# Kernel tuning notes

Measured on AMD Instinct MI355X. Metric: run time of the kernel, lower is better.

Reference implementation:

```python
import jax, jax.numpy as jnp
import numpy as np

SEQ_LEN, INPUT_DIM, HIDDEN_DIM, OUTPUT_DIM = 1024, 128, 256, 128
BATCH = 256


def setup_inputs() -> dict:
    key = jax.random.key(0)
    ks = jax.random.split(key, 7)
    s_ih = 1.0 / np.sqrt(INPUT_DIM)
    s_hh = 1.0 / np.sqrt(HIDDEN_DIM)
    return {
        "x": jax.random.normal(ks[0], (BATCH, SEQ_LEN, INPUT_DIM), jnp.float32),
        "W_ih": jax.random.normal(ks[1], (INPUT_DIM, 4 * HIDDEN_DIM), jnp.float32) * s_ih,
        "W_hh": jax.random.normal(ks[2], (HIDDEN_DIM, 4 * HIDDEN_DIM), jnp.float32) * s_hh,
        "b_ih": jax.random.normal(ks[3], (4 * HIDDEN_DIM,), jnp.float32) * s_hh,
        "b_hh": jax.random.normal(ks[4], (4 * HIDDEN_DIM,), jnp.float32) * s_hh,
        "W_out": jax.random.normal(ks[5], (HIDDEN_DIM, OUTPUT_DIM), jnp.float32) * s_hh,
        "b_out": jax.random.normal(ks[6], (OUTPUT_DIM,), jnp.float32) * s_hh,
    }


def reference(x, W_ih, W_hh, b_ih, b_hh, W_out, b_out):
    B, T, _ = x.shape
    H = W_hh.shape[0]
    # Precompute input projections for all timesteps: [T, B, 4H]
    x_proj = jnp.einsum("bti,ig->tbg", x, W_ih) + (b_ih + b_hh)

    def step(carry, xp_t):
        h, c = carry
        gates = xp_t + h @ W_hh  # [B, 4H]
        i_t, f_t, g_t, o_t = jnp.split(gates, 4, axis=1)
        i_t = jax.nn.sigmoid(i_t)
        f_t = jax.nn.sigmoid(f_t)
        g_t = jnp.tanh(g_t)
        o_t = jax.nn.sigmoid(o_t)
        c = f_t * c + i_t * g_t
        h = o_t * jnp.tanh(c)
        return (h, c), None

    h0 = jnp.zeros((B, H), x.dtype)
    c0 = jnp.zeros((B, H), x.dtype)
    (h_T, _), _ = jax.lax.scan(step, (h0, c0), x_proj)
    return h_T @ W_out + b_out
```

## Files before the change

### kernel.cpp

```cpp
#include <hip/hip_runtime.h>
#include <cstdint>


#define T_    1024
#define I_    128
#define H_    256

typedef short s8v __attribute__((ext_vector_type(8)));
typedef float f4v __attribute__((ext_vector_type(4)));
typedef unsigned short u16;
typedef unsigned int   u32;
typedef unsigned long long u64;

__device__ __forceinline__ u16 f2bf(float f) {
  union { float f; u32 u; } v; v.f = f;
  u32 r = v.u + 0x7FFFu + ((v.u >> 16) & 1u);
  return (u16)(r >> 16);
}
__device__ __forceinline__ float bf2f(u16 h) {
  union { u32 u; float f; } v; v.u = ((u32)h) << 16;
  return v.f;
}
__device__ __forceinline__ float sig_(float x)  { return 1.0f / (1.0f + __expf(-x)); }
__device__ __forceinline__ float tanh_(float x) { return 2.0f / (1.0f + __expf(-2.0f * x)) - 1.0f; }

__device__ __forceinline__ void unpack8(const u64 w[4], s8v& hi, s8v& lo) {
  #pragma unroll
  for (int j = 0; j < 4; j++) {
    u32 a = (u32)w[j], b = (u32)(w[j] >> 32);
    hi[2*j]   = (short)(u16)a;        lo[2*j]   = (short)(u16)(a >> 16);
    hi[2*j+1] = (short)(u16)b;        lo[2*j+1] = (short)(u16)(b >> 16);
  }
}

__device__ __forceinline__ bool tagok(u64 w, u32 tag) {
  return ((((u32)(w >> 16)) & 3u) == tag) & ((((u32)(w >> 48)) & 3u) == tag);
}

__device__ __forceinline__ void lgkm_barrier() {
  asm volatile("s_waitcnt lgkmcnt(0)" ::: "memory");
  __builtin_amdgcn_sched_barrier(0);
  __builtin_amdgcn_s_barrier();
  __builtin_amdgcn_sched_barrier(0);
  asm volatile("" ::: "memory");
}

__global__ __launch_bounds__(256, 1) void lstm_persist(
    const float* __restrict__ x, const float* __restrict__ Wih,
    const float* __restrict__ Whh, const float* __restrict__ bih,
    const float* __restrict__ bhh, const float* __restrict__ Wout,
    const float* __restrict__ bout, float* __restrict__ out,
    u32* __restrict__ flags, u32* __restrict__ hbuf)
{
  (void)flags;
  const int bid  = blockIdx.x;
  const int xcd  = bid & 7;
  const int slot = bid >> 3;
  const int ct   = slot & 15;
  const int g    = ((slot >> 4) << 3) | xcd;
  const int tid  = threadIdx.x;
  const int wave = tid >> 6;
  const int lane = tid & 63;
  const int lm   = lane & 15;
  const int lq   = lane >> 4;

  __shared__ u16   Wlds[2][64][392];
  __shared__ u16   xlds[2][2][16][136];
  __shared__ float partial[4][4][16][20];

  const int cm  = tid >> 4;
  const int chc = tid & 15;

  const size_t hpar   = (size_t)16 * 16 * 256;
  const size_t hgbase = (size_t)g * 16 * 256;

  {
    u32* hz = hbuf + hgbase + (size_t)cm * 256 + ct * 16 + chc;
    __hip_atomic_store(hz,        0x00010000u, __ATOMIC_RELAXED, __HIP_MEMORY_SCOPE_AGENT);
    __hip_atomic_store(hz + hpar, 0u,          __ATOMIC_RELAXED, __HIP_MEMORY_SCOPE_AGENT);
  }

  for (int it = tid; it < 384 * 64; it += 256) {
    int k = it >> 6;
    int c = it & 63;
    int gcol = (c >> 4) * 256 + ct * 16 + (c & 15);
    float w = (k < 128) ? Wih[k * 1024 + gcol] : Whh[(k - 128) * 1024 + gcol];
    u16 hi = f2bf(w);
    Wlds[0][c][k] = hi;
    Wlds[1][c][k] = f2bf(w - bf2f(hi));
  }
  __syncthreads();

  s8v wfrag[3][4][2];
  #pragma unroll
  for (int ki = 0; ki < 3; ki++) {
    const int kt = wave + 4 * ki;
    #pragma unroll
    for (int gg = 0; gg < 4; gg++) {
      #pragma unroll
      for (int p = 0; p < 2; p++)
        wfrag[ki][gg][p] = *(const s8v*)&Wlds[p][gg * 16 + lm][kt * 32 + lq * 8];
    }
  }
  __syncthreads();

  float biasv[4];
  #pragma unroll
  for (int gg = 0; gg < 4; gg++) {
    int col = gg * 256 + ct * 16 + chc;
    biasv[gg] = bih[col] + bhh[col];
  }
  float cstate = 0.0f;

  const int xr  = tid >> 4;
  const int xc0 = (tid & 15) * 8;
  const float* xbase = x + (size_t)(g * 16 + xr) * (T_ * I_) + xc0;

  auto xstore = [&](int par, float4 a, float4 b) {
    float v[8] = {a.x, a.y, a.z, a.w, b.x, b.y, b.z, b.w};
    union { u16 u[8]; s8v s; } hi, lo;
    #pragma unroll
    for (int j = 0; j < 8; j++) {
      u16 h = f2bf(v[j]);
      hi.u[j] = h;
      lo.u[j] = f2bf(v[j] - bf2f(h));
    }
    *(s8v*)&xlds[par][0][xr][xc0] = hi.s;
    *(s8v*)&xlds[par][1][xr][xc0] = lo.s;
  };

  {
    float4 a = *(const float4*)(xbase + 0);
    float4 b = *(const float4*)(xbase + 4);
    xstore(0, a, b);
  }
  __syncthreads();

  for (int t = 0; t < T_; t++) {
    const int par = t & 1;
    const int pn  = (t + 1) & 1;

    const int tn = (t + 1 < T_) ? (t + 1) : t;
    float4 xa = *(const float4*)(xbase + (size_t)tn * I_);
    float4 xb = *(const float4*)(xbase + (size_t)tn * I_ + 4);

    f4v acc[4];
    #pragma unroll
    for (int gg = 0; gg < 4; gg++)
      #pragma unroll
      for (int r = 0; r < 4; r++) acc[gg][r] = 0.0f;

    {
      s8v axh = *(const s8v*)&xlds[par][0][lm][wave * 32 + lq * 8];
      s8v axl = *(const s8v*)&xlds[par][1][lm][wave * 32 + lq * 8];
      #pragma unroll
      for (int gg = 0; gg < 4; gg++) {
        acc[gg] = __builtin_amdgcn_mfma_f32_16x16x32_bf16(axh, wfrag[0][gg][0], acc[gg], 0, 0, 0);
        acc[gg] = __builtin_amdgcn_mfma_f32_16x16x32_bf16(axl, wfrag[0][gg][0], acc[gg], 0, 0, 0);
        acc[gg] = __builtin_amdgcn_mfma_f32_16x16x32_bf16(axh, wfrag[0][gg][1], acc[gg], 0, 0, 0);
      }
    }

    if (t > 0) {
      const u32 tag = (u32)(t & 3);
      const u32* hb0 = hbuf + (size_t)par * hpar + hgbase;
      const u64* hp1 = (const u64*)(hb0 + (size_t)lm * 256 + (wave * 32 + lq * 8));
      const u64* hp2 = (const u64*)(hb0 + (size_t)lm * 256 + (wave * 32 + 128 + lq * 8));
      u64 w1[4], w2[4];
      while (true) {
        #pragma unroll
        for (int j = 0; j < 4; j++) {
          w1[j] = __hip_atomic_load(hp1 + j, __ATOMIC_RELAXED, __HIP_MEMORY_SCOPE_AGENT);
          w2[j] = __hip_atomic_load(hp2 + j, __ATOMIC_RELAXED, __HIP_MEMORY_SCOPE_AGENT);
        }
        bool ok = true;
        #pragma unroll
        for (int j = 0; j < 4; j++) {
          ok &= tagok(w1[j], tag);
          ok &= tagok(w2[j], tag);
        }
        if (__all(ok)) break;
        __builtin_amdgcn_s_sleep(1);
      }
      {
        s8v ahh, ahl;
        unpack8(w1, ahh, ahl);
        #pragma unroll
        for (int gg = 0; gg < 4; gg++) {
          acc[gg] = __builtin_amdgcn_mfma_f32_16x16x32_bf16(ahh, wfrag[1][gg][0], acc[gg], 0, 0, 0);
          acc[gg] = __builtin_amdgcn_mfma_f32_16x16x32_bf16(ahl, wfrag[1][gg][0], acc[gg], 0, 0, 0);
          acc[gg] = __builtin_amdgcn_mfma_f32_16x16x32_bf16(ahh, wfrag[1][gg][1], acc[gg], 0, 0, 0);
        }
        unpack8(w2, ahh, ahl);
        #pragma unroll
        for (int gg = 0; gg < 4; gg++) {
          acc[gg] = __builtin_amdgcn_mfma_f32_16x16x32_bf16(ahh, wfrag[2][gg][0], acc[gg], 0, 0, 0);
          acc[gg] = __builtin_amdgcn_mfma_f32_16x16x32_bf16(ahl, wfrag[2][gg][0], acc[gg], 0, 0, 0);
          acc[gg] = __builtin_amdgcn_mfma_f32_16x16x32_bf16(ahh, wfrag[2][gg][1], acc[gg], 0, 0, 0);
        }
      }
    }

    #pragma unroll
    for (int gg = 0; gg < 4; gg++)
      #pragma unroll
      for (int r = 0; r < 4; r++)
        partial[wave][gg][lq * 4 + r][lm] = acc[gg][r];

    xstore(pn, xa, xb);

    __syncthreads();

    float ga = biasv[0], gb = biasv[1], gc = biasv[2], gd = biasv[3];
    #pragma unroll
    for (int w = 0; w < 4; w++) {
      ga += partial[w][0][cm][chc];
      gb += partial[w][1][cm][chc];
      gc += partial[w][2][cm][chc];
      gd += partial[w][3][cm][chc];
    }
    float i_t = sig_(ga), f_t = sig_(gb), g_t = tanh_(gc), o_t = sig_(gd);
    cstate = f_t * cstate + i_t * g_t;
    float h = o_t * tanh_(cstate);

    u16 hhi = f2bf(h);
    u16 hlo = f2bf(h - bf2f(hhi));
    u32 pk  = ((u32)((hlo & 0xFFFCu) | (u32)((t + 1) & 3)) << 16) | (u32)hhi;
    u32* hw = hbuf + (size_t)pn * hpar + hgbase + (size_t)cm * 256 + ct * 16 + chc;
    __hip_atomic_store(hw, pk, __ATOMIC_RELAXED, __HIP_MEMORY_SCOPE_AGENT);

    lgkm_barrier();
  }

  u64 wf0[4], wf1[4];
  {
    const u32* hb0 = hbuf + hgbase;
    const u64* hpa = (const u64*)(hb0 + (size_t)lm * 256 + ((wave * 2 + 0) * 32 + lq * 8));
    const u64* hpb = (const u64*)(hb0 + (size_t)lm * 256 + ((wave * 2 + 1) * 32 + lq * 8));
    while (true) {
      #pragma unroll
      for (int j = 0; j < 4; j++) {
        wf0[j] = __hip_atomic_load(hpa + j, __ATOMIC_RELAXED, __HIP_MEMORY_SCOPE_AGENT);
        wf1[j] = __hip_atomic_load(hpb + j, __ATOMIC_RELAXED, __HIP_MEMORY_SCOPE_AGENT);
      }
      bool ok = true;
      #pragma unroll
      for (int j = 0; j < 4; j++) {
        ok &= tagok(wf0[j], 0u);
        ok &= tagok(wf1[j], 0u);
      }
      if (__all(ok)) break;
      __builtin_amdgcn_s_sleep(1);
    }
  }
  __syncthreads();
  for (int it = tid; it < 16 * 256; it += 256) {
    int n = it >> 8;
    int k = it & 255;
    float w = (n < 8) ? Wout[k * 128 + ct * 8 + n] : 0.0f;
    u16 hi = f2bf(w);
    Wlds[0][n][k] = hi;
    Wlds[1][n][k] = f2bf(w - bf2f(hi));
  }
  __syncthreads();

  f4v oacc;
  #pragma unroll
  for (int r = 0; r < 4; r++) oacc[r] = 0.0f;
  #pragma unroll
  for (int ki = 0; ki < 2; ki++) {
    const int hk = (wave * 2 + ki) * 32 + lq * 8;
    s8v ahh, ahl;
    unpack8(ki == 0 ? wf0 : wf1, ahh, ahl);
    s8v bh  = *(const s8v*)&Wlds[0][lm][hk];
    s8v bl  = *(const s8v*)&Wlds[1][lm][hk];
    oacc = __builtin_amdgcn_mfma_f32_16x16x32_bf16(ahh, bh, oacc, 0, 0, 0);
    oacc = __builtin_amdgcn_mfma_f32_16x16x32_bf16(ahl, bh, oacc, 0, 0, 0);
    oacc = __builtin_amdgcn_mfma_f32_16x16x32_bf16(ahh, bl, oacc, 0, 0, 0);
  }
  #pragma unroll
  for (int r = 0; r < 4; r++) partial[wave][0][lq * 4 + r][lm] = oacc[r];
  __syncthreads();

  if (tid < 128) {
    int m  = tid >> 3;
    int oc = tid & 7;
    float v = bout[ct * 8 + oc];
    #pragma unroll
    for (int w = 0; w < 4; w++) v += partial[w][0][m][oc];
    out[(size_t)(g * 16 + m) * 128 + ct * 8 + oc] = v;
  }
}

extern "C" void kernel_launch(void* const* d_in, const int* in_sizes, int n_in,
                              void* d_out, int out_size, void* d_ws, size_t ws_size,
                              hipStream_t stream) {
  const float* x    = (const float*)d_in[0];
  const float* Wih  = (const float*)d_in[1];
  const float* Whh  = (const float*)d_in[2];
  const float* bih  = (const float*)d_in[3];
  const float* bhh  = (const float*)d_in[4];
  const float* Wout = (const float*)d_in[5];
  const float* bout = (const float*)d_in[6];
  float* out = (float*)d_out;

  char* ws = (char*)d_ws;
  u32* flags = (u32*)ws;
  u32* hbuf  = (u32*)(ws + 4096);
  hipLaunchKernelGGL(lstm_persist, dim3(256), dim3(256), 0, stream,
                     x, Wih, Whh, bih, bhh, Wout, bout, out, flags, hbuf);
}
```

Measured before the change: 3.260 ms.

## Poll hidden state via XCC-local L2 when producer blocks share an XCC

```diff
diff --git a/kernel.cpp b/kernel.cpp
--- a/kernel.cpp
+++ b/kernel.cpp
@@ -35,6 +35,42 @@
 
 __device__ __forceinline__ bool tagok(u64 w, u32 tag) {
   return ((((u32)(w >> 16)) & 3u) == tag) & ((((u32)(w >> 48)) & 3u) == tag);
+}
+__device__ __forceinline__ int tags8(const u64* w1, const u64* w2, u32 tag) {
+  bool ok = true;
+  #pragma unroll
+  for (int j = 0; j < 4; j++) { ok &= tagok(w1[j], tag); ok &= tagok(w2[j], tag); }
+  return __all((int)ok);
+}
+
+#define POLL8_SC0(W1, W2, P1, P2)                                   \
+  asm volatile(                                                     \
+    "global_load_dwordx2 %0, %8, off offset:0 sc0\n\t"              \
+    "global_load_dwordx2 %1, %8, off offset:8 sc0\n\t"              \
+    "global_load_dwordx2 %2, %8, off offset:16 sc0\n\t"             \
+    "global_load_dwordx2 %3, %8, off offset:24 sc0\n\t"             \
+    "global_load_dwordx2 %4, %9, off offset:0 sc0\n\t"              \
+    "global_load_dwordx2 %5, %9, off offset:8 sc0\n\t"              \
+    "global_load_dwordx2 %6, %9, off offset:16 sc0\n\t"             \
+    "global_load_dwordx2 %7, %9, off offset:24 sc0\n\t"             \
+    "s_waitcnt vmcnt(0)"                                            \
+    : "=&v"(W1[0]), "=&v"(W1[1]), "=&v"(W1[2]), "=&v"(W1[3]),       \
+      "=&v"(W2[0]), "=&v"(W2[1]), "=&v"(W2[2]), "=&v"(W2[3])        \
+    : "v"(P1), "v"(P2) : "memory")
+
+#define POLL8_AGENT(W1, W2, A1, A2)                                           \
+  do {                                                                        \
+    _Pragma("unroll")                                                         \
+    for (int j_ = 0; j_ < 4; j_++) {                                          \
+      W1[j_] = __hip_atomic_load((A1) + j_, __ATOMIC_RELAXED,                 \
+                                 __HIP_MEMORY_SCOPE_AGENT);                   \
+      W2[j_] = __hip_atomic_load((A2) + j_, __ATOMIC_RELAXED,                 \
+                                 __HIP_MEMORY_SCOPE_AGENT);                   \
+    }                                                                         \
+  } while (0)
+
+__device__ __forceinline__ void store_wt(u32* p, u32 v) {
+  asm volatile("global_store_dword %0, %1, off sc0 sc1" :: "v"(p), "v"(v) : "memory");
 }
 
 __device__ __forceinline__ void lgkm_barrier() {
@@ -52,7 +88,6 @@
     const float* __restrict__ bout, float* __restrict__ out,
     u32* __restrict__ flags, u32* __restrict__ hbuf)
 {
-  (void)flags;
   const int bid  = blockIdx.x;
   const int xcd  = bid & 7;
   const int slot = bid >> 3;
@@ -74,10 +109,33 @@
   const size_t hpar   = (size_t)16 * 16 * 256;
   const size_t hgbase = (size_t)g * 16 * 256;
 
+  u32 xcc;
+  asm volatile("s_getreg_b32 %0, hwreg(HW_REG_XCC_ID)" : "=s"(xcc));
+  xcc &= 0xFu;
+  u32* xccmap = flags;
+  if (tid == 0)
+    __hip_atomic_store(&xccmap[bid], 0xC0DE0000u | xcc,
+                       __ATOMIC_RELAXED, __HIP_MEMORY_SCOPE_AGENT);
+  int spec;
+  {
+    int mok = 1;
+    if (lane < 16) {
+      const int pb = (g >> 3) * 128 + (lane & 15) * 8 + (g & 7);
+      u32 v;
+      while (true) {
+        v = __hip_atomic_load(&xccmap[pb], __ATOMIC_RELAXED, __HIP_MEMORY_SCOPE_AGENT);
+        if ((v >> 16) == 0xC0DEu) break;
+        __builtin_amdgcn_s_sleep(1);
+      }
+      mok = ((v & 0xFu) == xcc) ? 1 : 0;
+    }
+    spec = __all(mok);
+  }
+
   {
     u32* hz = hbuf + hgbase + (size_t)cm * 256 + ct * 16 + chc;
-    __hip_atomic_store(hz,        0x00010000u, __ATOMIC_RELAXED, __HIP_MEMORY_SCOPE_AGENT);
-    __hip_atomic_store(hz + hpar, 0u,          __ATOMIC_RELAXED, __HIP_MEMORY_SCOPE_AGENT);
+    store_wt(hz,        0x00010000u);
+    store_wt(hz + hpar, 0u);
   }
 
   for (int it = tid; it < 384 * 64; it += 256) {
@@ -164,22 +222,18 @@
     if (t > 0) {
       const u32 tag = (u32)(t & 3);
       const u32* hb0 = hbuf + (size_t)par * hpar + hgbase;
-      const u64* hp1 = (const u64*)(hb0 + (size_t)lm * 256 + (wave * 32 + lq * 8));
-      const u64* hp2 = (const u64*)(hb0 + (size_t)lm * 256 + (wave * 32 + 128 + lq * 8));
+      const u32* hp1 = hb0 + (size_t)lm * 256 + (wave * 32 + lq * 8);
+      const u32* hp2 = hp1 + 128;
+      const u64* a1 = (const u64*)hp1;
+      const u64* a2 = (const u64*)hp2;
       u64 w1[4], w2[4];
       while (true) {
-        #pragma unroll
-        for (int j = 0; j < 4; j++) {
-          w1[j] = __hip_atomic_load(hp1 + j, __ATOMIC_RELAXED, __HIP_MEMORY_SCOPE_AGENT);
-          w2[j] = __hip_atomic_load(hp2 + j, __ATOMIC_RELAXED, __HIP_MEMORY_SCOPE_AGENT);
+        if (spec) {
+          POLL8_SC0(w1, w2, hp1, hp2);
+          if (tags8(w1, w2, tag)) break;
         }
-        bool ok = true;
-        #pragma unroll
-        for (int j = 0; j < 4; j++) {
-          ok &= tagok(w1[j], tag);
-          ok &= tagok(w2[j], tag);
-        }
-        if (__all(ok)) break;
+        POLL8_AGENT(w1, w2, a1, a2);
+        if (tags8(w1, w2, tag)) break;
         __builtin_amdgcn_s_sleep(1);
       }
       {
@@ -227,7 +281,7 @@
     u16 hlo = f2bf(h - bf2f(hhi));
     u32 pk  = ((u32)((hlo & 0xFFFCu) | (u32)((t + 1) & 3)) << 16) | (u32)hhi;
     u32* hw = hbuf + (size_t)pn * hpar + hgbase + (size_t)cm * 256 + ct * 16 + chc;
-    __hip_atomic_store(hw, pk, __ATOMIC_RELAXED, __HIP_MEMORY_SCOPE_AGENT);
+    store_wt(hw, pk);
 
     lgkm_barrier();
   }
@@ -235,21 +289,17 @@
   u64 wf0[4], wf1[4];
   {
     const u32* hb0 = hbuf + hgbase;
-    const u64* hpa = (const u64*)(hb0 + (size_t)lm * 256 + ((wave * 2 + 0) * 32 + lq * 8));
-    const u64* hpb = (const u64*)(hb0 + (size_t)lm * 256 + ((wave * 2 + 1) * 32 + lq * 8));
+    const u32* hpa = hb0 + (size_t)lm * 256 + ((wave * 2 + 0) * 32 + lq * 8);
+    const u32* hpb = hpa + 32;
+    const u64* a1 = (const u64*)hpa;
+    const u64* a2 = (const u64*)hpb;
     while (true) {
-      #pragma unroll
-      for (int j = 0; j < 4; j++) {
-        wf0[j] = __hip_atomic_load(hpa + j, __ATOMIC_RELAXED, __HIP_MEMORY_SCOPE_AGENT);
-        wf1[j] = __hip_atomic_load(hpb + j, __ATOMIC_RELAXED, __HIP_MEMORY_SCOPE_AGENT);
-      }
-      bool ok = true;
-      #pragma unroll
-      for (int j = 0; j < 4; j++) {
-        ok &= tagok(wf0[j], 0u);
-        ok &= tagok(wf1[j], 0u);
-      }
-      if (__all(ok)) break;
+      if (spec) {
+        POLL8_SC0(wf0, wf1, hpa, hpb);
+        if (tags8(wf0, wf1, 0u)) break;
+      }
+      POLL8_AGENT(wf0, wf1, a1, a2);
+      if (tags8(wf0, wf1, 0u)) break;
       __builtin_amdgcn_s_sleep(1);
     }
   }
```

Result: faster. 3.195 ms (-2.0%).

## Double-buffer partial sums to drop one barrier per step and prefetch x two steps ahead

Applied to the files above, without the earlier changes.

```diff
diff --git a/kernel.cpp b/kernel.cpp
--- a/kernel.cpp
+++ b/kernel.cpp
@@ -36,6 +36,23 @@
 __device__ __forceinline__ bool tagok(u64 w, u32 tag) {
   return ((((u32)(w >> 16)) & 3u) == tag) & ((((u32)(w >> 48)) & 3u) == tag);
 }
+__device__ __forceinline__ int tags8(const u64* w1, const u64* w2, u32 tag) {
+  bool ok = true;
+  #pragma unroll
+  for (int j = 0; j < 4; j++) { ok &= tagok(w1[j], tag); ok &= tagok(w2[j], tag); }
+  return __all((int)ok);
+}
+
+#define POLL8_AGENT(W1, W2, A1, A2)                                           \
+  do {                                                                        \
+    _Pragma("unroll")                                                         \
+    for (int j_ = 0; j_ < 4; j_++) {                                          \
+      W1[j_] = __hip_atomic_load((A1) + j_, __ATOMIC_RELAXED,                 \
+                                 __HIP_MEMORY_SCOPE_AGENT);                   \
+      W2[j_] = __hip_atomic_load((A2) + j_, __ATOMIC_RELAXED,                 \
+                                 __HIP_MEMORY_SCOPE_AGENT);                   \
+    }                                                                         \
+  } while (0)
 
 __device__ __forceinline__ void lgkm_barrier() {
   asm volatile("s_waitcnt lgkmcnt(0)" ::: "memory");
@@ -66,7 +83,7 @@
 
   __shared__ u16   Wlds[2][64][392];
   __shared__ u16   xlds[2][2][16][136];
-  __shared__ float partial[4][4][16][20];
+  __shared__ float partial[2][4][4][16][20];
 
   const int cm  = tid >> 4;
   const int chc = tid & 15;
@@ -129,20 +146,23 @@
     *(s8v*)&xlds[par][1][xr][xc0] = lo.s;
   };
 
+  float4 xna, xnb, xfa, xfb;
   {
     float4 a = *(const float4*)(xbase + 0);
     float4 b = *(const float4*)(xbase + 4);
     xstore(0, a, b);
-  }
-  __syncthreads();
-
-  for (int t = 0; t < T_; t++) {
+    xna = *(const float4*)(xbase + (size_t)I_);
+    xnb = *(const float4*)(xbase + (size_t)I_ + 4);
+  }
+  __syncthreads();
+
+  auto step = [&](int t, float4& ra, float4& rb, float4& fa, float4& fb) {
     const int par = t & 1;
     const int pn  = (t + 1) & 1;
 
-    const int tn = (t + 1 < T_) ? (t + 1) : t;
-    float4 xa = *(const float4*)(xbase + (size_t)tn * I_);
-    float4 xb = *(const float4*)(xbase + (size_t)tn * I_ + 4);
+    const int tf = (t + 2 < T_) ? (t + 2) : (T_ - 1);
+    fa = *(const float4*)(xbase + (size_t)tf * I_);
+    fb = *(const float4*)(xbase + (size_t)tf * I_ + 4);
 
     f4v acc[4];
     #pragma unroll
@@ -164,22 +184,12 @@
     if (t > 0) {
       const u32 tag = (u32)(t & 3);
       const u32* hb0 = hbuf + (size_t)par * hpar + hgbase;
-      const u64* hp1 = (const u64*)(hb0 + (size_t)lm * 256 + (wave * 32 + lq * 8));
-      const u64* hp2 = (const u64*)(hb0 + (size_t)lm * 256 + (wave * 32 + 128 + lq * 8));
+      const u64* a1 = (const u64*)(hb0 + (size_t)lm * 256 + (wave * 32 + lq * 8));
+      const u64* a2 = (const u64*)(hb0 + (size_t)lm * 256 + (wave * 32 + 128 + lq * 8));
       u64 w1[4], w2[4];
       while (true) {
-        #pragma unroll
-        for (int j = 0; j < 4; j++) {
-          w1[j] = __hip_atomic_load(hp1 + j, __ATOMIC_RELAXED, __HIP_MEMORY_SCOPE_AGENT);
-          w2[j] = __hip_atomic_load(hp2 + j, __ATOMIC_RELAXED, __HIP_MEMORY_SCOPE_AGENT);
-        }
-        bool ok = true;
-        #pragma unroll
-        for (int j = 0; j < 4; j++) {
-          ok &= tagok(w1[j], tag);
-          ok &= tagok(w2[j], tag);
-        }
-        if (__all(ok)) break;
+        POLL8_AGENT(w1, w2, a1, a2);
+        if (tags8(w1, w2, tag)) break;
         __builtin_amdgcn_s_sleep(1);
       }
       {
@@ -205,19 +215,19 @@
     for (int gg = 0; gg < 4; gg++)
       #pragma unroll
       for (int r = 0; r < 4; r++)
-        partial[wave][gg][lq * 4 + r][lm] = acc[gg][r];
-
-    xstore(pn, xa, xb);
-
-    __syncthreads();
+        partial[par][wave][gg][lq * 4 + r][lm] = acc[gg][r];
+
+    xstore(pn, ra, rb);
+
+    lgkm_barrier();
 
     float ga = biasv[0], gb = biasv[1], gc = biasv[2], gd = biasv[3];
     #pragma unroll
     for (int w = 0; w < 4; w++) {
-      ga += partial[w][0][cm][chc];
-      gb += partial[w][1][cm][chc];
-      gc += partial[w][2][cm][chc];
-      gd += partial[w][3][cm][chc];
+      ga += partial[par][w][0][cm][chc];
+      gb += partial[par][w][1][cm][chc];
+      gc += partial[par][w][2][cm][chc];
+      gd += partial[par][w][3][cm][chc];
     }
     float i_t = sig_(ga), f_t = sig_(gb), g_t = tanh_(gc), o_t = sig_(gd);
     cstate = f_t * cstate + i_t * g_t;
@@ -228,28 +238,21 @@
     u32 pk  = ((u32)((hlo & 0xFFFCu) | (u32)((t + 1) & 3)) << 16) | (u32)hhi;
     u32* hw = hbuf + (size_t)pn * hpar + hgbase + (size_t)cm * 256 + ct * 16 + chc;
     __hip_atomic_store(hw, pk, __ATOMIC_RELAXED, __HIP_MEMORY_SCOPE_AGENT);
-
-    lgkm_barrier();
+  };
+
+  for (int t = 0; t < T_; t += 2) {
+    step(t,     xna, xnb, xfa, xfb);
+    step(t + 1, xfa, xfb, xna, xnb);
   }
 
   u64 wf0[4], wf1[4];
   {
     const u32* hb0 = hbuf + hgbase;
-    const u64* hpa = (const u64*)(hb0 + (size_t)lm * 256 + ((wave * 2 + 0) * 32 + lq * 8));
-    const u64* hpb = (const u64*)(hb0 + (size_t)lm * 256 + ((wave * 2 + 1) * 32 + lq * 8));
+    const u64* a1 = (const u64*)(hb0 + (size_t)lm * 256 + ((wave * 2 + 0) * 32 + lq * 8));
+    const u64* a2 = (const u64*)(hb0 + (size_t)lm * 256 + ((wave * 2 + 1) * 32 + lq * 8));
     while (true) {
-      #pragma unroll
-      for (int j = 0; j < 4; j++) {
-        wf0[j] = __hip_atomic_load(hpa + j, __ATOMIC_RELAXED, __HIP_MEMORY_SCOPE_AGENT);
-        wf1[j] = __hip_atomic_load(hpb + j, __ATOMIC_RELAXED, __HIP_MEMORY_SCOPE_AGENT);
-      }
-      bool ok = true;
-      #pragma unroll
-      for (int j = 0; j < 4; j++) {
-        ok &= tagok(wf0[j], 0u);
-        ok &= tagok(wf1[j], 0u);
-      }
-      if (__all(ok)) break;
+      POLL8_AGENT(wf0, wf1, a1, a2);
+      if (tags8(wf0, wf1, 0u)) break;
       __builtin_amdgcn_s_sleep(1);
     }
   }
@@ -279,7 +282,7 @@
     oacc = __builtin_amdgcn_mfma_f32_16x16x32_bf16(ahh, bl, oacc, 0, 0, 0);
   }
   #pragma unroll
-  for (int r = 0; r < 4; r++) partial[wave][0][lq * 4 + r][lm] = oacc[r];
+  for (int r = 0; r < 4; r++) partial[0][wave][0][lq * 4 + r][lm] = oacc[r];
   __syncthreads();
 
   if (tid < 128) {
@@ -287,7 +290,7 @@
     int oc = tid & 7;
     float v = bout[ct * 8 + oc];
     #pragma unroll
-    for (int w = 0; w < 4; w++) v += partial[w][0][m][oc];
+    for (int w = 0; w < 4; w++) v += partial[0][w][0][m][oc];
     out[(size_t)(g * 16 + m) * 128 + ct * 8 + oc] = v;
   }
 }
```

Measured after the change: 3.823 ms. 1.17x slower.
